# Optimization experiments

Hardware: AMD Instinct MI355X
Metric: run time of the kernel (lower is better)

The kernel has to match this reference:

```python
import jax, jax.numpy as jnp
import numpy as np

N_NODES = 50000


def setup_inputs() -> dict:
    key = jax.random.key(0)
    k1, k2, k3 = jax.random.split(key, 3)
    x = jax.random.normal(k1, (N_NODES, 256), dtype=jnp.float32)
    edge_index = jax.random.randint(k2, (2, 1600000), 0, N_NODES, dtype=jnp.int64)
    W = jax.random.normal(k3, (256, 256), dtype=jnp.float32) / np.sqrt(256.0)
    b = jnp.zeros((256,), dtype=jnp.float32)
    return {"x": x, "edge_index": edge_index, "W": W, "b": b}


def reference(x, edge_index, W, b):
    # PyG GCNConv: add self-loops, symmetric normalization, linear, aggregate, bias; then ReLU.
    n = x.shape[0]
    self_loops = jnp.arange(n, dtype=edge_index.dtype)
    src = jnp.concatenate([edge_index[0], self_loops])  # [E+N]
    dst = jnp.concatenate([edge_index[1], self_loops])  # [E+N]

    # degree from incoming edges (incl. self loops)
    deg = jax.ops.segment_sum(jnp.ones_like(dst, dtype=x.dtype), dst, num_segments=n)
    dinv = jnp.where(deg > 0, jax.lax.rsqrt(deg), 0.0)
    norm = dinv[src] * dinv[dst]  # [E+N]

    xw = x @ W  # [N, out] linear first (GCNConv transforms then propagates)
    msgs = xw[src] * norm[:, None]  # gather + edge-normalize
    agg = jax.ops.segment_sum(msgs, dst, num_segments=n)  # scatter-add
    return jax.nn.relu(agg + b)
```

## Files before the change

### kernel.cpp

```cpp
#include <hip/hip_runtime.h>
#include <hip/hip_bf16.h>


#define FEATS 256
#define MAXBUCK 200
#define P1_CAP 64
#define BCAP 10240

typedef __bf16 bf16x8 __attribute__((ext_vector_type(8)));
typedef float f32x4 __attribute__((ext_vector_type(4)));

__device__ __forceinline__ unsigned short f2bf(float f) {
  unsigned u = __float_as_uint(f);
  u += 0x7fffu + ((u >> 16) & 1u);
  return (unsigned short)(u >> 16);
}
__device__ __forceinline__ float bflo(unsigned u) { return __uint_as_float(u << 16); }
__device__ __forceinline__ float bfhi(unsigned u) { return __uint_as_float(u & 0xFFFF0000u); }


__global__ __launch_bounds__(256) void zero_i32(int* __restrict__ p, int n) {
  int i = blockIdx.x * 256 + threadIdx.x;
  if (i < n) p[i] = 0;
}

__global__ __launch_bounds__(1024) void pass1_bin(const int* __restrict__ src,
                                                  const int* __restrict__ dst,
                                                  int E, int nbuck,
                                                  int* __restrict__ gcursor,
                                                  unsigned* __restrict__ temp) {
  __shared__ unsigned lbuf[MAXBUCK * P1_CAP];
  __shared__ int lcnt[MAXBUCK];
  __shared__ int lbase[MAXBUCK];
  const int tid = threadIdx.x;
  for (int i = tid; i < nbuck; i += 1024) lcnt[i] = 0;
  __syncthreads();

  const int e0 = blockIdx.x * 4096;
  #pragma unroll
  for (int i = 0; i < 4; ++i) {
    int e = e0 + i * 1024 + tid;
    if (e < E) {
      unsigned d = (unsigned)dst[e];
      unsigned p = (d << 16) | (unsigned)src[e];
      int b = (int)(d >> 8);
      int pos = atomicAdd(&lcnt[b], 1);
      if (pos < P1_CAP) {
        lbuf[b * P1_CAP + pos] = p;
      } else {
        int gp = atomicAdd(&gcursor[b], 1);
        temp[(size_t)b * BCAP + gp] = p;
      }
    }
  }
  __syncthreads();
  if (tid < nbuck) {
    int c = lcnt[tid]; if (c > P1_CAP) c = P1_CAP;
    lcnt[tid] = c;
    lbase[tid] = atomicAdd(&gcursor[tid], c);
  }
  __syncthreads();
  for (int i = tid; i < nbuck * P1_CAP; i += 1024) {
    int b = i >> 6, j = i & (P1_CAP - 1);
    if (j < lcnt[b]) temp[(size_t)b * BCAP + lbase[b] + j] = lbuf[i];
  }
}

__global__ __launch_bounds__(256) void scan_buckets(const int* __restrict__ gcursor,
                                                    int* __restrict__ bbase,
                                                    int* __restrict__ row_ptr,
                                                    int nbuck, int n) {
  __shared__ int tmp[256];
  int t = threadIdx.x;
  int v = (t < nbuck) ? min(gcursor[t], BCAP) : 0;
  tmp[t] = v;
  __syncthreads();
  #pragma unroll
  for (int off = 1; off < 256; off <<= 1) {
    int x = (t >= off) ? tmp[t - off] : 0;
    __syncthreads();
    tmp[t] += x;
    __syncthreads();
  }
  if (t < nbuck) bbase[t] = tmp[t] - v;
  if (t == 0) row_ptr[n] = tmp[255];
}

__global__ __launch_bounds__(1024) void pass2_csr(const unsigned* __restrict__ temp,
                                                  const int* __restrict__ gcursor,
                                                  const int* __restrict__ bbase,
                                                  unsigned short* __restrict__ csr16,
                                                  int* __restrict__ row_ptr,
                                                  float* __restrict__ dinv, int n) {
  __shared__ unsigned ebuf[BCAP];
  __shared__ unsigned short sorted[BCAP];
  __shared__ int hist[256], scn[256], sexcl[256], ofs[256];
  const int b = blockIdx.x;
  const int tid = threadIdx.x;
  int cnt = gcursor[b]; if (cnt > BCAP) cnt = BCAP;
  const int base = bbase[b];
  const unsigned* tp = temp + (size_t)b * BCAP;

  if (tid < 256) { hist[tid] = 0; ofs[tid] = 0; }
  for (int i = tid; i < cnt; i += 1024) ebuf[i] = tp[i];
  __syncthreads();
  for (int i = tid; i < cnt; i += 1024) atomicAdd(&hist[(ebuf[i] >> 16) & 255], 1);
  __syncthreads();

  if (tid < 256) scn[tid] = hist[tid];
  __syncthreads();
  #pragma unroll
  for (int off = 1; off < 256; off <<= 1) {
    int x = 0;
    if (tid < 256 && tid >= off) x = scn[tid - off];
    __syncthreads();
    if (tid < 256) scn[tid] += x;
    __syncthreads();
  }
  if (tid < 256) {
    int v = hist[tid];
    int excl = scn[tid] - v;
    sexcl[tid] = excl;
    int node = (b << 8) + tid;
    if (node < n) {
      row_ptr[node] = base + excl;
      dinv[node] = rsqrtf((float)(v + 1));
    }
  }
  __syncthreads();

  for (int i = tid; i < cnt; i += 1024) {
    unsigned e = ebuf[i];
    int dl = (int)((e >> 16) & 255);
    int pos = sexcl[dl] + atomicAdd(&ofs[dl], 1);
    sorted[pos] = (unsigned short)(e & 0xFFFFu);
  }
  __syncthreads();
  for (int i = tid; i < cnt; i += 1024) csr16[base + i] = sorted[i];
}


__global__ __launch_bounds__(256) void wt_build(const float* __restrict__ W,
                                                unsigned short* __restrict__ Wt) {
  int k = blockIdx.x;
  int nn = threadIdx.x;
  Wt[nn * FEATS + k] = f2bf(W[k * FEATS + nn]);
}


__global__ __launch_bounds__(256, 2) void gemm_mfma(const float* __restrict__ x,
                                                    const unsigned short* __restrict__ Wt,
                                                    const float* __restrict__ dinv,
                                                    unsigned short* __restrict__ xwp, int M) {
  __shared__ bf16x8 A_lds[32 * 64];
  const int wv   = (int)(threadIdx.x >> 6);
  const int lane = (int)(threadIdx.x & 63);
  const int lm   = lane & 15;
  const int quad = lane >> 4;
  const int m0   = (int)blockIdx.x * 64;

  bf16x8 Bfrag[4][8];
  #pragma unroll
  for (int ct = 0; ct < 4; ++ct) {
    const unsigned short* wrow = Wt + (size_t)(wv * 64 + ct * 16 + lm) * FEATS + quad * 8;
    #pragma unroll
    for (int kc = 0; kc < 8; ++kc)
      Bfrag[ct][kc] = *(const bf16x8*)(wrow + kc * 32);
  }

  {
    int arow = m0 + wv * 16 + lm; if (arow >= M) arow = M - 1;
    const float* xrow = x + (size_t)arow * FEATS + quad * 8;
    #pragma unroll
    for (int kc = 0; kc < 8; ++kc) {
      const float4 f0 = *(const float4*)(xrow + kc * 32);
      const float4 f1 = *(const float4*)(xrow + kc * 32 + 4);
      union { bf16x8 v; unsigned short u[8]; } a;
      a.u[0] = f2bf(f0.x); a.u[1] = f2bf(f0.y); a.u[2] = f2bf(f0.z); a.u[3] = f2bf(f0.w);
      a.u[4] = f2bf(f1.x); a.u[5] = f2bf(f1.y); a.u[6] = f2bf(f1.z); a.u[7] = f2bf(f1.w);
      A_lds[(wv * 8 + kc) * 64 + lane] = a.v;
    }
  }
  __syncthreads();

  #pragma unroll
  for (int sub = 0; sub < 4; ++sub) {
    bf16x8 Af[8];
    #pragma unroll
    for (int kc = 0; kc < 8; ++kc) Af[kc] = A_lds[(sub * 8 + kc) * 64 + lane];

    f32x4 acc[4];
    #pragma unroll
    for (int ct = 0; ct < 4; ++ct) acc[ct] = (f32x4){0.f, 0.f, 0.f, 0.f};

    #pragma unroll
    for (int kc = 0; kc < 8; ++kc) {
      #pragma unroll
      for (int ct = 0; ct < 4; ++ct)
        acc[ct] = __builtin_amdgcn_mfma_f32_16x16x32_bf16(Af[kc], Bfrag[ct][kc], acc[ct], 0, 0, 0);
    }

    #pragma unroll
    for (int r = 0; r < 4; ++r) {
      const int row = m0 + sub * 16 + quad * 4 + r;
      if (row < M) {
        const float dd = dinv[row];
        unsigned short* orow = xwp + (size_t)row * FEATS + wv * 64 + lm;
        #pragma unroll
        for (int ct = 0; ct < 4; ++ct)
          orow[ct * 16] = f2bf(acc[ct][r] * dd);
      }
    }
  }
}


__global__ __launch_bounds__(256) void aggregate(const unsigned short* __restrict__ xwp,
                                                 const float* __restrict__ dinv,
                                                 const int* __restrict__ row_ptr,
                                                 const unsigned short* __restrict__ csr16,
                                                 const float* __restrict__ bias,
                                                 float* __restrict__ out, int n) {
  const int node = (int)((blockIdx.x * blockDim.x + threadIdx.x) >> 6);
  const int lane = (int)(threadIdx.x & 63);
  if (node >= n) return;
  const int co = lane << 2;

  uint2 sv = *(const uint2*)(xwp + (((size_t)node) << 8) + co);
  float4 acc;
  acc.x = bflo(sv.x); acc.y = bfhi(sv.x); acc.z = bflo(sv.y); acc.w = bfhi(sv.y);

  const int beg = row_ptr[node];
  const int end = row_ptr[node + 1];
  for (int base = beg; base < end; base += 64) {
    int idx = base + lane;
    int s = (idx < end) ? (int)csr16[idx] : 0;
    int m = end - base;
    if (m > 64) m = 64;
    int i = 0;
    for (; i + 8 <= m; i += 8) {
      uint2 v[8];
      #pragma unroll
      for (int j = 0; j < 8; ++j) {
        int sj = __shfl(s, i + j);
        v[j] = *(const uint2*)(xwp + (((size_t)sj) << 8) + co);
      }
      #pragma unroll
      for (int j = 0; j < 8; ++j) {
        acc.x += bflo(v[j].x); acc.y += bfhi(v[j].x);
        acc.z += bflo(v[j].y); acc.w += bfhi(v[j].y);
      }
    }
    for (; i < m; ++i) {
      int sj = __shfl(s, i);
      uint2 v = *(const uint2*)(xwp + (((size_t)sj) << 8) + co);
      acc.x += bflo(v.x); acc.y += bfhi(v.x);
      acc.z += bflo(v.y); acc.w += bfhi(v.y);
    }
  }

  const float dd = dinv[node];
  const float* bp = bias + co;
  f32x4 o;
  o.x = fmaxf(fmaf(acc.x, dd, bp[0]), 0.f);
  o.y = fmaxf(fmaf(acc.y, dd, bp[1]), 0.f);
  o.z = fmaxf(fmaf(acc.z, dd, bp[2]), 0.f);
  o.w = fmaxf(fmaf(acc.w, dd, bp[3]), 0.f);
  __builtin_nontemporal_store(o, (f32x4*)(out + (((size_t)node) << 8) + co));
}


extern "C" void kernel_launch(void* const* d_in, const int* in_sizes, int n_in,
                              void* d_out, int out_size, void* d_ws, size_t ws_size,
                              hipStream_t stream) {
  const float* x  = (const float*)d_in[0];
  const int*   ei = (const int*)d_in[1];
  const float* W  = (const float*)d_in[2];
  const float* b  = (const float*)d_in[3];

  const int n = in_sizes[0] / FEATS;
  const int E = in_sizes[1] / 2;
  const int* src = ei;
  const int* dst = ei + E;
  const int nbuck = (n + 255) >> 8;

  char* ws = (char*)d_ws;
  unsigned short* xwp   = (unsigned short*)(ws);
  unsigned short* Wt    = (unsigned short*)(ws + 25600000);
  float*          dinv  = (float*)(ws + 25731072);
  int*            row_ptr = (int*)(ws + 25931072);
  unsigned short* csr16 = (unsigned short*)(ws + 26131136);
  int*            gcursor = (int*)(ws + 29331136);
  int*            bbase   = (int*)(ws + 29332160);
  unsigned*       temp    = (unsigned*)(ws + 29333184);

  hipLaunchKernelGGL(zero_i32, dim3(1), dim3(256), 0, stream, gcursor, nbuck);
  hipLaunchKernelGGL(wt_build, dim3(256), dim3(256), 0, stream, W, Wt);

  const int g_p1 = (E + 4095) / 4096;
  hipLaunchKernelGGL(pass1_bin, dim3(g_p1), dim3(1024), 0, stream, src, dst, E, nbuck, gcursor, temp);
  hipLaunchKernelGGL(scan_buckets, dim3(1), dim3(256), 0, stream, gcursor, bbase, row_ptr, nbuck, n);
  hipLaunchKernelGGL(pass2_csr, dim3(nbuck), dim3(1024), 0, stream, temp, gcursor, bbase,
                     csr16, row_ptr, dinv, n);

  hipLaunchKernelGGL(gemm_mfma, dim3((n + 63) / 64), dim3(256), 0, stream, x, Wt, dinv, xwp, n);

  const int g_agg = (n * 64 + 255) / 256;
  hipLaunchKernelGGL(aggregate, dim3(g_agg), dim3(256), 0, stream,
                     xwp, dinv, row_ptr, csr16, b, (float*)d_out, n);
}
```

Baseline: 256.2 us.

## Slice xw into 32-column panels and aggregate per slice for cache locality

The GEMM now writes xw in a column-sliced layout (8 slices of 32 bf16 columns, each covering all nodes plus one zeroed pad row). Aggregation runs as two launches of four slices each. Each wave handles one node and one slice, with eight edge groups gathering 64-byte rows in parallel and a shuffle reduction at the end. The goal is to keep each slice's gather working set small enough to stay in cache, so random-gather traffic drops. In exchange, the edge indices and row_ptr are read eight times over, and there are more blocks and cross-lane reductions.

```diff
diff --git a/kernel.cpp b/kernel.cpp
--- a/kernel.cpp
+++ b/kernel.cpp
@@ -19,10 +19,17 @@
 __device__ __forceinline__ float bfhi(unsigned u) { return __uint_as_float(u & 0xFFFF0000u); }
 
 
-__global__ __launch_bounds__(256) void zero_i32(int* __restrict__ p, int n) {
-  int i = blockIdx.x * 256 + threadIdx.x;
-  if (i < n) p[i] = 0;
-}
+__global__ __launch_bounds__(512) void init_misc(int* __restrict__ gcursor, int nbuck,
+                                                 int* __restrict__ xwp_i, int npad, int n) {
+  const int t = threadIdx.x;
+  if (t < nbuck) gcursor[t] = 0;
+  const int j = t - 256;
+  if (j >= 0 && j < 128) {
+    const int s = j >> 4, w = j & 15;
+    xwp_i[((size_t)s * npad + n) * 16 + w] = 0;
+  }
+}
+
 
 __global__ __launch_bounds__(1024) void pass1_bin(const int* __restrict__ src,
                                                   const int* __restrict__ dst,
@@ -151,7 +158,8 @@
 __global__ __launch_bounds__(256, 2) void gemm_mfma(const float* __restrict__ x,
                                                     const unsigned short* __restrict__ Wt,
                                                     const float* __restrict__ dinv,
-                                                    unsigned short* __restrict__ xwp, int M) {
+                                                    unsigned short* __restrict__ xwp,
+                                                    int M, int npad) {
   __shared__ bf16x8 A_lds[32 * 64];
   const int wv   = (int)(threadIdx.x >> 6);
   const int lane = (int)(threadIdx.x & 63);
@@ -205,10 +213,12 @@
       const int row = m0 + sub * 16 + quad * 4 + r;
       if (row < M) {
         const float dd = dinv[row];
-        unsigned short* orow = xwp + (size_t)row * FEATS + wv * 64 + lm;
         #pragma unroll
-        for (int ct = 0; ct < 4; ++ct)
-          orow[ct * 16] = f2bf(acc[ct][r] * dd);
+        for (int ct = 0; ct < 4; ++ct) {
+          const int c = wv * 64 + ct * 16 + lm;
+          const int sl = c >> 5, off = c & 31;
+          xwp[((size_t)sl * npad + row) * 32 + off] = f2bf(acc[ct][r] * dd);
+        }
       }
     }
   }
@@ -220,53 +230,61 @@
                                                  const int* __restrict__ row_ptr,
                                                  const unsigned short* __restrict__ csr16,
                                                  const float* __restrict__ bias,
-                                                 float* __restrict__ out, int n) {
-  const int node = (int)((blockIdx.x * blockDim.x + threadIdx.x) >> 6);
+                                                 float* __restrict__ out,
+                                                 int n, int npad, int nbps, int sl0) {
+  const int sl   = sl0 + (int)(blockIdx.x / nbps);
+  const int node = ((int)(blockIdx.x % nbps)) * 4 + (int)(threadIdx.x >> 6);
   const int lane = (int)(threadIdx.x & 63);
   if (node >= n) return;
-  const int co = lane << 2;
-
-  uint2 sv = *(const uint2*)(xwp + (((size_t)node) << 8) + co);
-  float4 acc;
-  acc.x = bflo(sv.x); acc.y = bfhi(sv.x); acc.z = bflo(sv.y); acc.w = bfhi(sv.y);
+  const int eg = lane >> 3;
+  const int cl = lane & 7;
+  const unsigned short* xs = xwp + (size_t)sl * npad * 32 + cl * 4;
+
+  float4 acc = {0.f, 0.f, 0.f, 0.f};
+  if (eg == 0) {
+    uint2 v = *(const uint2*)(xs + (size_t)node * 32);
+    acc.x = bflo(v.x); acc.y = bfhi(v.x); acc.z = bflo(v.y); acc.w = bfhi(v.y);
+  }
 
   const int beg = row_ptr[node];
   const int end = row_ptr[node + 1];
   for (int base = beg; base < end; base += 64) {
     int idx = base + lane;
-    int s = (idx < end) ? (int)csr16[idx] : 0;
-    int m = end - base;
-    if (m > 64) m = 64;
-    int i = 0;
-    for (; i + 8 <= m; i += 8) {
-      uint2 v[8];
-      #pragma unroll
-      for (int j = 0; j < 8; ++j) {
-        int sj = __shfl(s, i + j);
-        v[j] = *(const uint2*)(xwp + (((size_t)sj) << 8) + co);
-      }
-      #pragma unroll
-      for (int j = 0; j < 8; ++j) {
-        acc.x += bflo(v[j].x); acc.y += bfhi(v[j].x);
-        acc.z += bflo(v[j].y); acc.w += bfhi(v[j].y);
-      }
-    }
-    for (; i < m; ++i) {
-      int sj = __shfl(s, i);
-      uint2 v = *(const uint2*)(xwp + (((size_t)sj) << 8) + co);
-      acc.x += bflo(v.x); acc.y += bfhi(v.x);
-      acc.z += bflo(v.y); acc.w += bfhi(v.y);
-    }
+    int sb = (idx < end) ? (int)csr16[idx] : n;
+    int m = end - base; if (m > 64) m = 64;
+    for (int i = 0; i < m; i += 32) {
+      int s0 = __shfl(sb, i + eg);
+      int s1 = __shfl(sb, i + 8 + eg);
+      int s2 = __shfl(sb, i + 16 + eg);
+      int s3 = __shfl(sb, i + 24 + eg);
+      uint2 v0 = *(const uint2*)(xs + (size_t)s0 * 32);
+      uint2 v1 = *(const uint2*)(xs + (size_t)s1 * 32);
+      uint2 v2 = *(const uint2*)(xs + (size_t)s2 * 32);
+      uint2 v3 = *(const uint2*)(xs + (size_t)s3 * 32);
+      acc.x += bflo(v0.x); acc.y += bfhi(v0.x); acc.z += bflo(v0.y); acc.w += bfhi(v0.y);
+      acc.x += bflo(v1.x); acc.y += bfhi(v1.x); acc.z += bflo(v1.y); acc.w += bfhi(v1.y);
+      acc.x += bflo(v2.x); acc.y += bfhi(v2.x); acc.z += bflo(v2.y); acc.w += bfhi(v2.y);
+      acc.x += bflo(v3.x); acc.y += bfhi(v3.x); acc.z += bflo(v3.y); acc.w += bfhi(v3.y);
+    }
+  }
+
+  #pragma unroll
+  for (int st = 8; st < 64; st <<= 1) {
+    acc.x += __shfl_xor(acc.x, st);
+    acc.y += __shfl_xor(acc.y, st);
+    acc.z += __shfl_xor(acc.z, st);
+    acc.w += __shfl_xor(acc.w, st);
   }
 
   const float dd = dinv[node];
-  const float* bp = bias + co;
+  const float4 bb = *(const float4*)(bias + sl * 32 + cl * 4);
   f32x4 o;
-  o.x = fmaxf(fmaf(acc.x, dd, bp[0]), 0.f);
-  o.y = fmaxf(fmaf(acc.y, dd, bp[1]), 0.f);
-  o.z = fmaxf(fmaf(acc.z, dd, bp[2]), 0.f);
-  o.w = fmaxf(fmaf(acc.w, dd, bp[3]), 0.f);
-  __builtin_nontemporal_store(o, (f32x4*)(out + (((size_t)node) << 8) + co));
+  o.x = fmaxf(fmaf(acc.x, dd, bb.x), 0.f);
+  o.y = fmaxf(fmaf(acc.y, dd, bb.y), 0.f);
+  o.z = fmaxf(fmaf(acc.z, dd, bb.z), 0.f);
+  o.w = fmaxf(fmaf(acc.w, dd, bb.w), 0.f);
+  if (eg == 0)
+    __builtin_nontemporal_store(o, (f32x4*)(out + (size_t)node * 256 + sl * 32 + cl * 4));
 }
 
 
@@ -283,18 +301,20 @@
   const int* src = ei;
   const int* dst = ei + E;
   const int nbuck = (n + 255) >> 8;
+  const int npad = n + 1;
 
   char* ws = (char*)d_ws;
-  unsigned short* xwp   = (unsigned short*)(ws);
-  unsigned short* Wt    = (unsigned short*)(ws + 25600000);
-  float*          dinv  = (float*)(ws + 25731072);
-  int*            row_ptr = (int*)(ws + 25931072);
-  unsigned short* csr16 = (unsigned short*)(ws + 26131136);
-  int*            gcursor = (int*)(ws + 29331136);
-  int*            bbase   = (int*)(ws + 29332160);
-  unsigned*       temp    = (unsigned*)(ws + 29333184);
-
-  hipLaunchKernelGGL(zero_i32, dim3(1), dim3(256), 0, stream, gcursor, nbuck);
+  size_t o0 = 0;
+  unsigned short* xwp   = (unsigned short*)(ws + o0); o0 += (size_t)npad * 512;
+  unsigned short* Wt    = (unsigned short*)(ws + o0); o0 += 131072;
+  float*          dinv  = (float*)(ws + o0);          o0 += 200064;
+  int*            row_ptr = (int*)(ws + o0);          o0 += 200064;
+  unsigned short* csr16 = (unsigned short*)(ws + o0); o0 += 3200000;
+  int*            gcursor = (int*)(ws + o0);          o0 += 1024;
+  int*            bbase   = (int*)(ws + o0);          o0 += 1024;
+  unsigned*       temp    = (unsigned*)(ws + o0);     o0 += (size_t)nbuck * BCAP * 4;
+
+  hipLaunchKernelGGL(init_misc, dim3(1), dim3(512), 0, stream, gcursor, nbuck, (int*)xwp, npad, n);
   hipLaunchKernelGGL(wt_build, dim3(256), dim3(256), 0, stream, W, Wt);
 
   const int g_p1 = (E + 4095) / 4096;
@@ -303,9 +323,11 @@
   hipLaunchKernelGGL(pass2_csr, dim3(nbuck), dim3(1024), 0, stream, temp, gcursor, bbase,
                      csr16, row_ptr, dinv, n);
 
-  hipLaunchKernelGGL(gemm_mfma, dim3((n + 63) / 64), dim3(256), 0, stream, x, Wt, dinv, xwp, n);
-
-  const int g_agg = (n * 64 + 255) / 256;
-  hipLaunchKernelGGL(aggregate, dim3(g_agg), dim3(256), 0, stream,
-                     xwp, dinv, row_ptr, csr16, b, (float*)d_out, n);
-}
+  hipLaunchKernelGGL(gemm_mfma, dim3((n + 63) / 64), dim3(256), 0, stream, x, Wt, dinv, xwp, n, npad);
+
+  const int nbps = (n + 3) / 4;
+  hipLaunchKernelGGL(aggregate, dim3(nbps * 4), dim3(256), 0, stream,
+                     xwp, dinv, row_ptr, csr16, b, (float*)d_out, n, npad, nbps, 0);
+  hipLaunchKernelGGL(aggregate, dim3(nbps * 4), dim3(256), 0, stream,
+                     xwp, dinv, row_ptr, csr16, b, (float*)d_out, n, npad, nbps, 4);
+}
```

After: 307.4 us. 20.0% more time.

## Build CSR with global-atomic counting sort and split aggregation into four launches

Applied to the files above, without the earlier changes.

Replaces the bucketed two-pass shared-memory binning (pass1_bin/pass2_csr) with a plain counting sort: global atomic degree count, three-stage prefix scan, then an atomic-cursor scatter of source indices into the CSR. It also splits the aggregate kernel into four sequential launches over node quarters. This removes the fixed bucket capacity and the large temp buffer, but the scatter now relies on global atomics and produces a nondeterministic neighbor order within each row. The extra launches add launch overhead, and it is unclear what the quarter split is meant to gain.

```diff
diff --git a/kernel.cpp b/kernel.cpp
--- a/kernel.cpp
+++ b/kernel.cpp
@@ -3,9 +3,6 @@
 
 
 #define FEATS 256
-#define MAXBUCK 200
-#define P1_CAP 64
-#define BCAP 10240
 
 typedef __bf16 bf16x8 __attribute__((ext_vector_type(8)));
 typedef float f32x4 __attribute__((ext_vector_type(4)));
@@ -24,55 +21,20 @@
   if (i < n) p[i] = 0;
 }
 
-__global__ __launch_bounds__(1024) void pass1_bin(const int* __restrict__ src,
-                                                  const int* __restrict__ dst,
-                                                  int E, int nbuck,
-                                                  int* __restrict__ gcursor,
-                                                  unsigned* __restrict__ temp) {
-  __shared__ unsigned lbuf[MAXBUCK * P1_CAP];
-  __shared__ int lcnt[MAXBUCK];
-  __shared__ int lbase[MAXBUCK];
-  const int tid = threadIdx.x;
-  for (int i = tid; i < nbuck; i += 1024) lcnt[i] = 0;
-  __syncthreads();
-
-  const int e0 = blockIdx.x * 4096;
-  #pragma unroll
-  for (int i = 0; i < 4; ++i) {
-    int e = e0 + i * 1024 + tid;
-    if (e < E) {
-      unsigned d = (unsigned)dst[e];
-      unsigned p = (d << 16) | (unsigned)src[e];
-      int b = (int)(d >> 8);
-      int pos = atomicAdd(&lcnt[b], 1);
-      if (pos < P1_CAP) {
-        lbuf[b * P1_CAP + pos] = p;
-      } else {
-        int gp = atomicAdd(&gcursor[b], 1);
-        temp[(size_t)b * BCAP + gp] = p;
-      }
-    }
-  }
-  __syncthreads();
-  if (tid < nbuck) {
-    int c = lcnt[tid]; if (c > P1_CAP) c = P1_CAP;
-    lcnt[tid] = c;
-    lbase[tid] = atomicAdd(&gcursor[tid], c);
-  }
-  __syncthreads();
-  for (int i = tid; i < nbuck * P1_CAP; i += 1024) {
-    int b = i >> 6, j = i & (P1_CAP - 1);
-    if (j < lcnt[b]) temp[(size_t)b * BCAP + lbase[b] + j] = lbuf[i];
-  }
-}
-
-__global__ __launch_bounds__(256) void scan_buckets(const int* __restrict__ gcursor,
-                                                    int* __restrict__ bbase,
-                                                    int* __restrict__ row_ptr,
-                                                    int nbuck, int n) {
+__global__ __launch_bounds__(256) void count_deg(const int* __restrict__ dst, int E,
+                                                 int* __restrict__ deg) {
+  int e = blockIdx.x * 256 + threadIdx.x;
+  if (e < E) atomicAdd(&deg[dst[e]], 1);
+}
+
+__global__ __launch_bounds__(256) void scanA(const int* __restrict__ deg,
+                                             int* __restrict__ row_ptr,
+                                             float* __restrict__ dinv,
+                                             int* __restrict__ bsum, int n) {
   __shared__ int tmp[256];
-  int t = threadIdx.x;
-  int v = (t < nbuck) ? min(gcursor[t], BCAP) : 0;
+  const int t = threadIdx.x;
+  const int i = blockIdx.x * 256 + t;
+  const int v = (i < n) ? deg[i] : 0;
   tmp[t] = v;
   __syncthreads();
   #pragma unroll
@@ -82,61 +44,53 @@
     tmp[t] += x;
     __syncthreads();
   }
-  if (t < nbuck) bbase[t] = tmp[t] - v;
-  if (t == 0) row_ptr[n] = tmp[255];
-}
-
-__global__ __launch_bounds__(1024) void pass2_csr(const unsigned* __restrict__ temp,
-                                                  const int* __restrict__ gcursor,
-                                                  const int* __restrict__ bbase,
-                                                  unsigned short* __restrict__ csr16,
-                                                  int* __restrict__ row_ptr,
-                                                  float* __restrict__ dinv, int n) {
-  __shared__ unsigned ebuf[BCAP];
-  __shared__ unsigned short sorted[BCAP];
-  __shared__ int hist[256], scn[256], sexcl[256], ofs[256];
-  const int b = blockIdx.x;
-  const int tid = threadIdx.x;
-  int cnt = gcursor[b]; if (cnt > BCAP) cnt = BCAP;
-  const int base = bbase[b];
-  const unsigned* tp = temp + (size_t)b * BCAP;
-
-  if (tid < 256) { hist[tid] = 0; ofs[tid] = 0; }
-  for (int i = tid; i < cnt; i += 1024) ebuf[i] = tp[i];
+  if (i < n) {
+    row_ptr[i] = tmp[t] - v;
+    dinv[i] = rsqrtf((float)(v + 1));
+  }
+  if (t == 255) bsum[blockIdx.x] = tmp[255];
+}
+
+__global__ __launch_bounds__(256) void scanB(int* __restrict__ bsum, int nb,
+                                             int* __restrict__ row_ptr, int n) {
+  __shared__ int tmp[256];
+  const int t = threadIdx.x;
+  const int v = (t < nb) ? bsum[t] : 0;
+  tmp[t] = v;
   __syncthreads();
-  for (int i = tid; i < cnt; i += 1024) atomicAdd(&hist[(ebuf[i] >> 16) & 255], 1);
-  __syncthreads();
-
-  if (tid < 256) scn[tid] = hist[tid];
-  __syncthreads();
   #pragma unroll
   for (int off = 1; off < 256; off <<= 1) {
-    int x = 0;
-    if (tid < 256 && tid >= off) x = scn[tid - off];
-    __syncthreads();
-    if (tid < 256) scn[tid] += x;
-    __syncthreads();
-  }
-  if (tid < 256) {
-    int v = hist[tid];
-    int excl = scn[tid] - v;
-    sexcl[tid] = excl;
-    int node = (b << 8) + tid;
-    if (node < n) {
-      row_ptr[node] = base + excl;
-      dinv[node] = rsqrtf((float)(v + 1));
-    }
-  }
-  __syncthreads();
-
-  for (int i = tid; i < cnt; i += 1024) {
-    unsigned e = ebuf[i];
-    int dl = (int)((e >> 16) & 255);
-    int pos = sexcl[dl] + atomicAdd(&ofs[dl], 1);
-    sorted[pos] = (unsigned short)(e & 0xFFFFu);
-  }
-  __syncthreads();
-  for (int i = tid; i < cnt; i += 1024) csr16[base + i] = sorted[i];
+    int x = (t >= off) ? tmp[t - off] : 0;
+    __syncthreads();
+    tmp[t] += x;
+    __syncthreads();
+  }
+  if (t < nb) bsum[t] = tmp[t] - v;
+  if (t == nb - 1) row_ptr[n] = tmp[t];
+}
+
+__global__ __launch_bounds__(256) void scanC(int* __restrict__ row_ptr,
+                                             const int* __restrict__ bsum,
+                                             int* __restrict__ cursor, int n) {
+  const int i = blockIdx.x * 256 + threadIdx.x;
+  if (i < n) {
+    const int r = row_ptr[i] + bsum[blockIdx.x];
+    row_ptr[i] = r;
+    cursor[i] = r;
+  }
+}
+
+__global__ __launch_bounds__(256) void fill_csr(const int* __restrict__ src,
+                                                const int* __restrict__ dst, int E,
+                                                int* __restrict__ cursor,
+                                                unsigned short* __restrict__ csr16) {
+  int e = blockIdx.x * 256 + threadIdx.x;
+  if (e < E) {
+    const int d = dst[e];
+    const int s = src[e];
+    const int pos = atomicAdd(&cursor[d], 1);
+    csr16[pos] = (unsigned short)s;
+  }
 }
 
 
@@ -220,10 +174,11 @@
                                                  const int* __restrict__ row_ptr,
                                                  const unsigned short* __restrict__ csr16,
                                                  const float* __restrict__ bias,
-                                                 float* __restrict__ out, int n) {
-  const int node = (int)((blockIdx.x * blockDim.x + threadIdx.x) >> 6);
+                                                 float* __restrict__ out,
+                                                 int n0, int n1) {
+  const int node = n0 + (int)((blockIdx.x * blockDim.x + threadIdx.x) >> 6);
   const int lane = (int)(threadIdx.x & 63);
-  if (node >= n) return;
+  if (node >= n1) return;
   const int co = lane << 2;
 
   uint2 sv = *(const uint2*)(xwp + (((size_t)node) << 8) + co);
@@ -282,30 +237,36 @@
   const int E = in_sizes[1] / 2;
   const int* src = ei;
   const int* dst = ei + E;
-  const int nbuck = (n + 255) >> 8;
+  const int nsb = (n + 255) >> 8;
 
   char* ws = (char*)d_ws;
-  unsigned short* xwp   = (unsigned short*)(ws);
-  unsigned short* Wt    = (unsigned short*)(ws + 25600000);
-  float*          dinv  = (float*)(ws + 25731072);
-  int*            row_ptr = (int*)(ws + 25931072);
-  unsigned short* csr16 = (unsigned short*)(ws + 26131136);
-  int*            gcursor = (int*)(ws + 29331136);
-  int*            bbase   = (int*)(ws + 29332160);
-  unsigned*       temp    = (unsigned*)(ws + 29333184);
-
-  hipLaunchKernelGGL(zero_i32, dim3(1), dim3(256), 0, stream, gcursor, nbuck);
+  size_t o0 = 0;
+  unsigned short* xwp    = (unsigned short*)(ws + o0); o0 += (size_t)n * 512;
+  unsigned short* Wt     = (unsigned short*)(ws + o0); o0 += 131072;
+  float*          dinv   = (float*)(ws + o0);          o0 += 200064;
+  int*            row_ptr = (int*)(ws + o0);           o0 += 200064;
+  int*            deg    = (int*)(ws + o0);            o0 += 200064;
+  int*            cursor = (int*)(ws + o0);            o0 += 200064;
+  int*            bsum   = (int*)(ws + o0);            o0 += 1024;
+  unsigned short* csr16  = (unsigned short*)(ws + o0); o0 += 3200000;
+
+  hipLaunchKernelGGL(zero_i32, dim3(nsb), dim3(256), 0, stream, deg, n);
   hipLaunchKernelGGL(wt_build, dim3(256), dim3(256), 0, stream, W, Wt);
 
-  const int g_p1 = (E + 4095) / 4096;
-  hipLaunchKernelGGL(pass1_bin, dim3(g_p1), dim3(1024), 0, stream, src, dst, E, nbuck, gcursor, temp);
-  hipLaunchKernelGGL(scan_buckets, dim3(1), dim3(256), 0, stream, gcursor, bbase, row_ptr, nbuck, n);
-  hipLaunchKernelGGL(pass2_csr, dim3(nbuck), dim3(1024), 0, stream, temp, gcursor, bbase,
-                     csr16, row_ptr, dinv, n);
+  const int g_e = (E + 255) / 256;
+  hipLaunchKernelGGL(count_deg, dim3(g_e), dim3(256), 0, stream, dst, E, deg);
+  hipLaunchKernelGGL(scanA, dim3(nsb), dim3(256), 0, stream, deg, row_ptr, dinv, bsum, n);
+  hipLaunchKernelGGL(scanB, dim3(1), dim3(256), 0, stream, bsum, nsb, row_ptr, n);
+  hipLaunchKernelGGL(scanC, dim3(nsb), dim3(256), 0, stream, row_ptr, bsum, cursor, n);
+  hipLaunchKernelGGL(fill_csr, dim3(g_e), dim3(256), 0, stream, src, dst, E, cursor, csr16);
 
   hipLaunchKernelGGL(gemm_mfma, dim3((n + 63) / 64), dim3(256), 0, stream, x, Wt, dinv, xwp, n);
 
-  const int g_agg = (n * 64 + 255) / 256;
-  hipLaunchKernelGGL(aggregate, dim3(g_agg), dim3(256), 0, stream,
-                     xwp, dinv, row_ptr, csr16, b, (float*)d_out, n);
-}
+  int qb[5];
+  for (int q = 0; q <= 4; ++q) qb[q] = (int)(((long long)n * q) / 4);
+  for (int q = 0; q < 4; ++q) {
+    const int nn = qb[q + 1] - qb[q];
+    hipLaunchKernelGGL(aggregate, dim3((nn * 64 + 255) / 256), dim3(256), 0, stream,
+                       xwp, dinv, row_ptr, csr16, b, (float*)d_out, qb[q], qb[q + 1]);
+  }
+}
```

Measured after the change: 438.8 us. +71.3%, slower.

## Halve CSR build bucket size to double pass2 blocks; split aggregate into quarters

Applied to the files above, without the earlier changes.

Each destination bucket now covers 128 nodes instead of 256, so there are 391 buckets. pass2_csr therefore launches about twice as many blocks, each using less shared memory, which should spread the CSR sort over more CUs. The aggregate kernel is also split into four sequential launches over node ranges, presumably to improve cache locality of the gathered rows or to probe launch behaviour. The costs are more per-block overhead in pass1, a larger scan, and three extra kernel launches.

```diff
diff --git a/kernel.cpp b/kernel.cpp
--- a/kernel.cpp
+++ b/kernel.cpp
@@ -3,9 +3,9 @@
 
 
 #define FEATS 256
-#define MAXBUCK 200
-#define P1_CAP 64
-#define BCAP 10240
+#define NBUCK 391
+#define P1_CAP 32
+#define BCAP 5120
 
 typedef __bf16 bf16x8 __attribute__((ext_vector_type(8)));
 typedef float f32x4 __attribute__((ext_vector_type(4)));
@@ -26,14 +26,14 @@
 
 __global__ __launch_bounds__(1024) void pass1_bin(const int* __restrict__ src,
                                                   const int* __restrict__ dst,
-                                                  int E, int nbuck,
+                                                  int E,
                                                   int* __restrict__ gcursor,
                                                   unsigned* __restrict__ temp) {
-  __shared__ unsigned lbuf[MAXBUCK * P1_CAP];
-  __shared__ int lcnt[MAXBUCK];
-  __shared__ int lbase[MAXBUCK];
+  __shared__ unsigned lbuf[NBUCK * P1_CAP];
+  __shared__ int lcnt[NBUCK];
+  __shared__ int lbase[NBUCK];
   const int tid = threadIdx.x;
-  for (int i = tid; i < nbuck; i += 1024) lcnt[i] = 0;
+  for (int i = tid; i < NBUCK; i += 1024) lcnt[i] = 0;
   __syncthreads();
 
   const int e0 = blockIdx.x * 4096;
@@ -43,7 +43,7 @@
     if (e < E) {
       unsigned d = (unsigned)dst[e];
       unsigned p = (d << 16) | (unsigned)src[e];
-      int b = (int)(d >> 8);
+      int b = (int)(d >> 7);
       int pos = atomicAdd(&lcnt[b], 1);
       if (pos < P1_CAP) {
         lbuf[b * P1_CAP + pos] = p;
@@ -54,36 +54,36 @@
     }
   }
   __syncthreads();
-  if (tid < nbuck) {
+  if (tid < NBUCK) {
     int c = lcnt[tid]; if (c > P1_CAP) c = P1_CAP;
     lcnt[tid] = c;
     lbase[tid] = atomicAdd(&gcursor[tid], c);
   }
   __syncthreads();
-  for (int i = tid; i < nbuck * P1_CAP; i += 1024) {
-    int b = i >> 6, j = i & (P1_CAP - 1);
+  for (int i = tid; i < NBUCK * P1_CAP; i += 1024) {
+    int b = i >> 5, j = i & (P1_CAP - 1);
     if (j < lcnt[b]) temp[(size_t)b * BCAP + lbase[b] + j] = lbuf[i];
   }
 }
 
-__global__ __launch_bounds__(256) void scan_buckets(const int* __restrict__ gcursor,
+__global__ __launch_bounds__(512) void scan_buckets(const int* __restrict__ gcursor,
                                                     int* __restrict__ bbase,
                                                     int* __restrict__ row_ptr,
-                                                    int nbuck, int n) {
-  __shared__ int tmp[256];
+                                                    int n) {
+  __shared__ int tmp[512];
   int t = threadIdx.x;
-  int v = (t < nbuck) ? min(gcursor[t], BCAP) : 0;
+  int v = (t < NBUCK) ? min(gcursor[t], BCAP) : 0;
   tmp[t] = v;
   __syncthreads();
   #pragma unroll
-  for (int off = 1; off < 256; off <<= 1) {
+  for (int off = 1; off < 512; off <<= 1) {
     int x = (t >= off) ? tmp[t - off] : 0;
     __syncthreads();
     tmp[t] += x;
     __syncthreads();
   }
-  if (t < nbuck) bbase[t] = tmp[t] - v;
-  if (t == 0) row_ptr[n] = tmp[255];
+  if (t < NBUCK) bbase[t] = tmp[t] - v;
+  if (t == 511) row_ptr[n] = tmp[511];
 }
 
 __global__ __launch_bounds__(1024) void pass2_csr(const unsigned* __restrict__ temp,
@@ -94,34 +94,34 @@
                                                   float* __restrict__ dinv, int n) {
   __shared__ unsigned ebuf[BCAP];
   __shared__ unsigned short sorted[BCAP];
-  __shared__ int hist[256], scn[256], sexcl[256], ofs[256];
+  __shared__ int hist[128], scn[128], sexcl[128], ofs[128];
   const int b = blockIdx.x;
   const int tid = threadIdx.x;
   int cnt = gcursor[b]; if (cnt > BCAP) cnt = BCAP;
   const int base = bbase[b];
   const unsigned* tp = temp + (size_t)b * BCAP;
 
-  if (tid < 256) { hist[tid] = 0; ofs[tid] = 0; }
+  if (tid < 128) { hist[tid] = 0; ofs[tid] = 0; }
   for (int i = tid; i < cnt; i += 1024) ebuf[i] = tp[i];
   __syncthreads();
-  for (int i = tid; i < cnt; i += 1024) atomicAdd(&hist[(ebuf[i] >> 16) & 255], 1);
-  __syncthreads();
-
-  if (tid < 256) scn[tid] = hist[tid];
-  __syncthreads();
-  #pragma unroll
-  for (int off = 1; off < 256; off <<= 1) {
+  for (int i = tid; i < cnt; i += 1024) atomicAdd(&hist[(ebuf[i] >> 16) & 127], 1);
+  __syncthreads();
+
+  if (tid < 128) scn[tid] = hist[tid];
+  __syncthreads();
+  #pragma unroll
+  for (int off = 1; off < 128; off <<= 1) {
     int x = 0;
-    if (tid < 256 && tid >= off) x = scn[tid - off];
+    if (tid < 128 && tid >= off) x = scn[tid - off];
     __syncthreads();
-    if (tid < 256) scn[tid] += x;
+    if (tid < 128) scn[tid] += x;
     __syncthreads();
   }
-  if (tid < 256) {
+  if (tid < 128) {
     int v = hist[tid];
     int excl = scn[tid] - v;
     sexcl[tid] = excl;
-    int node = (b << 8) + tid;
+    int node = (b << 7) + tid;
     if (node < n) {
       row_ptr[node] = base + excl;
       dinv[node] = rsqrtf((float)(v + 1));
@@ -131,7 +131,7 @@
 
   for (int i = tid; i < cnt; i += 1024) {
     unsigned e = ebuf[i];
-    int dl = (int)((e >> 16) & 255);
+    int dl = (int)((e >> 16) & 127);
     int pos = sexcl[dl] + atomicAdd(&ofs[dl], 1);
     sorted[pos] = (unsigned short)(e & 0xFFFFu);
   }
@@ -220,10 +220,11 @@
                                                  const int* __restrict__ row_ptr,
                                                  const unsigned short* __restrict__ csr16,
                                                  const float* __restrict__ bias,
-                                                 float* __restrict__ out, int n) {
-  const int node = (int)((blockIdx.x * blockDim.x + threadIdx.x) >> 6);
+                                                 float* __restrict__ out,
+                                                 int n0, int n1) {
+  const int node = n0 + (int)((blockIdx.x * blockDim.x + threadIdx.x) >> 6);
   const int lane = (int)(threadIdx.x & 63);
-  if (node >= n) return;
+  if (node >= n1) return;
   const int co = lane << 2;
 
   uint2 sv = *(const uint2*)(xwp + (((size_t)node) << 8) + co);
@@ -282,30 +283,34 @@
   const int E = in_sizes[1] / 2;
   const int* src = ei;
   const int* dst = ei + E;
-  const int nbuck = (n + 255) >> 8;
 
   char* ws = (char*)d_ws;
-  unsigned short* xwp   = (unsigned short*)(ws);
-  unsigned short* Wt    = (unsigned short*)(ws + 25600000);
-  float*          dinv  = (float*)(ws + 25731072);
-  int*            row_ptr = (int*)(ws + 25931072);
-  unsigned short* csr16 = (unsigned short*)(ws + 26131136);
-  int*            gcursor = (int*)(ws + 29331136);
-  int*            bbase   = (int*)(ws + 29332160);
-  unsigned*       temp    = (unsigned*)(ws + 29333184);
-
-  hipLaunchKernelGGL(zero_i32, dim3(1), dim3(256), 0, stream, gcursor, nbuck);
+  size_t o0 = 0;
+  unsigned short* xwp    = (unsigned short*)(ws + o0); o0 += (size_t)n * 512;
+  unsigned short* Wt     = (unsigned short*)(ws + o0); o0 += 131072;
+  float*          dinv   = (float*)(ws + o0);          o0 += 200064;
+  int*            row_ptr = (int*)(ws + o0);           o0 += 200064;
+  unsigned short* csr16  = (unsigned short*)(ws + o0); o0 += 3200000;
+  int*            gcursor = (int*)(ws + o0);           o0 += 2048;
+  int*            bbase   = (int*)(ws + o0);           o0 += 2048;
+  unsigned*       temp    = (unsigned*)(ws + o0);      o0 += (size_t)NBUCK * BCAP * 4;
+
+  hipLaunchKernelGGL(zero_i32, dim3(2), dim3(256), 0, stream, gcursor, NBUCK);
   hipLaunchKernelGGL(wt_build, dim3(256), dim3(256), 0, stream, W, Wt);
 
   const int g_p1 = (E + 4095) / 4096;
-  hipLaunchKernelGGL(pass1_bin, dim3(g_p1), dim3(1024), 0, stream, src, dst, E, nbuck, gcursor, temp);
-  hipLaunchKernelGGL(scan_buckets, dim3(1), dim3(256), 0, stream, gcursor, bbase, row_ptr, nbuck, n);
-  hipLaunchKernelGGL(pass2_csr, dim3(nbuck), dim3(1024), 0, stream, temp, gcursor, bbase,
+  hipLaunchKernelGGL(pass1_bin, dim3(g_p1), dim3(1024), 0, stream, src, dst, E, gcursor, temp);
+  hipLaunchKernelGGL(scan_buckets, dim3(1), dim3(512), 0, stream, gcursor, bbase, row_ptr, n);
+  hipLaunchKernelGGL(pass2_csr, dim3(NBUCK), dim3(1024), 0, stream, temp, gcursor, bbase,
                      csr16, row_ptr, dinv, n);
 
   hipLaunchKernelGGL(gemm_mfma, dim3((n + 63) / 64), dim3(256), 0, stream, x, Wt, dinv, xwp, n);
 
-  const int g_agg = (n * 64 + 255) / 256;
-  hipLaunchKernelGGL(aggregate, dim3(g_agg), dim3(256), 0, stream,
-                     xwp, dinv, row_ptr, csr16, b, (float*)d_out, n);
-}
+  int qb[5];
+  for (int q = 0; q <= 4; ++q) qb[q] = (int)(((long long)n * q) / 4);
+  for (int q = 0; q < 4; ++q) {
+    const int nn = qb[q + 1] - qb[q];
+    hipLaunchKernelGGL(aggregate, dim3((nn * 64 + 255) / 256), dim3(256), 0, stream,
+                       xwp, dinv, row_ptr, csr16, b, (float*)d_out, qb[q], qb[q + 1]);
+  }
+}
```

Result: slower. 271.6 us (+6.0%).
